# Performance work log

Measured on AMD Instinct MI355X. Metric: run time of the kernel, lower is better.

## Reference

```python
import jax, jax.numpy as jnp
import numpy as np

B, S, D, H, HD, L, V, FF = 4, 2048, 768, 12, 64, 6, 32000, 3072
EPS = 1e-5


def setup_inputs() -> dict:
    key = jax.random.key(0)
    ks = jax.random.split(key, 12)
    s = 0.02
    return {
        "input_ids": jax.random.randint(ks[0], (B, S), 0, V),
        "emb": jax.random.normal(ks[1], (V, D), jnp.float32) * s,
        "q_w": jax.random.normal(ks[2], (L, D, D), jnp.float32) * s,
        "q_b": jnp.zeros((L, D), jnp.float32),
        "k_w": jax.random.normal(ks[3], (L, D, D), jnp.float32) * s,
        "k_b": jnp.zeros((L, D), jnp.float32),
        "v_w": jax.random.normal(ks[4], (L, D, D), jnp.float32) * s,
        "v_b": jnp.zeros((L, D), jnp.float32),
        "o_w": jax.random.normal(ks[5], (L, D, D), jnp.float32) * s,
        "o_b": jnp.zeros((L, D), jnp.float32),
        "f1_w": jax.random.normal(ks[6], (L, D, FF), jnp.float32) * s,
        "f1_b": jnp.zeros((L, FF), jnp.float32),
        "f2_w": jax.random.normal(ks[7], (L, FF, D), jnp.float32) * s,
        "f2_b": jnp.zeros((L, D), jnp.float32),
        "n1_w": jnp.ones((L, D), jnp.float32),
        "n1_b": jnp.zeros((L, D), jnp.float32),
        "n2_w": jnp.ones((L, D), jnp.float32),
        "n2_b": jnp.zeros((L, D), jnp.float32),
        "fn_w": jnp.ones((D,), jnp.float32),
        "fn_b": jnp.zeros((D,), jnp.float32),
    }


def _ln(x, w, b):
    m = jnp.mean(x, axis=-1, keepdims=True)
    v = jnp.var(x, axis=-1, keepdims=True)
    return (x - m) * jax.lax.rsqrt(v + EPS) * w + b


def _rope(x):
    # x: [B, S, D]; RoPE applied on full embed dim (as in source)
    inv_freq = 1.0 / (10000.0 ** (jnp.arange(0, D, 2, dtype=jnp.float32) / D))
    ang = jnp.arange(x.shape[1], dtype=jnp.float32)[:, None] * inv_freq[None, :]  # [S, D/2]
    cos, sin = jnp.cos(ang), jnp.sin(ang)
    xe, xo = x[..., ::2], x[..., 1::2]
    re = xe * cos - xo * sin
    ro = xo * cos + xe * sin
    return jnp.stack([re, ro], axis=-1).reshape(x.shape)


def _forward(input_ids, emb, q_w, q_b, k_w, k_b, v_w, v_b, o_w, o_b,
             f1_w, f1_b, f2_w, f2_b, n1_w, n1_b, n2_w, n2_b, fn_w, fn_b):
    h = _rope(emb[input_ids])  # [B, S, D]
    scale = 1.0 / np.sqrt(HD)

    def block(h, p):
        (qw, qb, kw, kb, vw, vb, ow, ob, f1w, f1b, f2w, f2b,
         w1, b1, w2, b2) = p
        xn = _ln(h, w1, b1)
        q = (xn @ qw + qb).reshape(B, S, H, HD)
        k = (xn @ kw + kb).reshape(B, S, H, HD)
        v = (xn @ vw + vb).reshape(B, S, H, HD)
        scores = jnp.einsum('bqhd,bkhd->bhqk', q, k) * scale
        attn = jax.nn.softmax(scores, axis=-1)
        ctx = jnp.einsum('bhqk,bkhd->bqhd', attn, v).reshape(B, S, D)
        h = h + (ctx @ ow + ob)
        xn2 = _ln(h, w2, b2)
        ff = jax.nn.gelu(xn2 @ f1w + f1b, approximate=False) @ f2w + f2b
        return h + ff, None

    params = (q_w, q_b, k_w, k_b, v_w, v_b, o_w, o_b,
              f1_w, f1_b, f2_w, f2_b, n1_w, n1_b, n2_w, n2_b)
    h, _ = jax.lax.scan(block, h, params)
    h = _ln(h, fn_w, fn_b)
    return h @ emb.T  # tied output projection: [B, S, V]


def reference(input_ids, emb, q_w, q_b, k_w, k_b, v_w, v_b, o_w, o_b,
              f1_w, f1_b, f2_w, f2_b, n1_w, n1_b, n2_w, n2_b, fn_w, fn_b):
    return _forward(input_ids, emb, q_w, q_b, k_w, k_b, v_w, v_b, o_w, o_b,
                    f1_w, f1_b, f2_w, f2_b, n1_w, n1_b, n2_w, n2_b, fn_w, fn_b)
```

## Files before the change

kernel.cpp:

```cpp
#include <hip/hip_runtime.h>
#include <hip/hip_bf16.h>
#include <cstdint>
#include <cstddef>

#define TB 4
#define TS 2048
#define TD 768
#define TH 12
#define THD 64
#define TL 6
#define TV 32000
#define TFF 3072
#define TT (TB*TS)
#define TQKV 2304

typedef __bf16 bf16_t;
typedef __attribute__((ext_vector_type(8))) __bf16 bf16x8;
typedef __attribute__((ext_vector_type(4))) __bf16 bf16x4;
typedef __attribute__((ext_vector_type(4))) float f32x4;

__device__ __forceinline__ unsigned short f2bf(float f) {
  union { float f; unsigned u; } x; x.f = f;
  unsigned r = x.u + 0x7fffu + ((x.u >> 16) & 1u);
  return (unsigned short)(r >> 16);
}

__device__ __forceinline__ float fexp2(float x) {
  float r; asm("v_exp_f32 %0, %1" : "=v"(r) : "v"(x)); return r;
}

__device__ __forceinline__ void gld_lds16(const void* g, void* l) {
  unsigned loff = (unsigned)(uintptr_t)l;
  __builtin_amdgcn_global_load_lds(
      (const __attribute__((address_space(1))) unsigned int*)(uintptr_t)g,
      (__attribute__((address_space(3))) unsigned int*)(uintptr_t)loff, 16, 0, 0);
}

#define IRFENCE() asm volatile("" ::: "memory")

__global__ void embed_rope(const int* __restrict__ ids, const float* __restrict__ emb,
                           float* __restrict__ h) {
  int t = blockIdx.x;
  int s = t & (TS - 1);
  int id = ids[t];
  const float* row = emb + (size_t)id * TD;
  float* out = h + (size_t)t * TD;
  for (int p = threadIdx.x; p < TD/2; p += blockDim.x) {
    float xe = row[2*p], xo = row[2*p+1];
    float inv = expf(-(float)(2*p) * (9.210340371976184f / (float)TD));
    float ang = (float)s * inv;
    float c = cosf(ang), sn = sinf(ang);
    out[2*p]   = xe*c - xo*sn;
    out[2*p+1] = xo*c + xe*sn;
  }
}

__global__ __launch_bounds__(256) void ln_fwd(const float* __restrict__ x,
                                              const float* __restrict__ w,
                                              const float* __restrict__ b,
                                              unsigned short* __restrict__ y) {
  int row = blockIdx.x;
  const float* xr = x + (size_t)row * TD;
  int tid = threadIdx.x;
  float4 v = {0.f, 0.f, 0.f, 0.f};
  if (tid < 192) v = *(const float4*)(xr + tid*4);
  float s = (v.x+v.y)+(v.z+v.w);
  float q = (v.x*v.x+v.y*v.y)+(v.z*v.z+v.w*v.w);
  for (int o = 32; o; o >>= 1) { s += __shfl_down(s, o); q += __shfl_down(q, o); }
  __shared__ float ss[4], sq[4];
  int wave = tid >> 6, lane = tid & 63;
  if (lane == 0) { ss[wave] = s; sq[wave] = q; }
  __syncthreads();
  s = ss[0]+ss[1]+ss[2]+ss[3];
  q = sq[0]+sq[1]+sq[2]+sq[3];
  float mean = s * (1.0f/TD);
  float var  = q * (1.0f/TD) - mean*mean;
  float rstd = rsqrtf(var + 1e-5f);
  if (tid < 192) {
    const float4 wv = *(const float4*)(w + tid*4);
    const float4 bv = *(const float4*)(b + tid*4);
    ushort4 o4;
    o4.x = f2bf((v.x-mean)*rstd*wv.x + bv.x);
    o4.y = f2bf((v.y-mean)*rstd*wv.y + bv.y);
    o4.z = f2bf((v.z-mean)*rstd*wv.z + bv.z);
    o4.w = f2bf((v.w-mean)*rstd*wv.w + bv.w);
    *(ushort4*)(y + (size_t)row*TD + tid*4) = o4;
  }
}

__global__ __launch_bounds__(256) void transpose_to_bf16(const float* __restrict__ W,
                                                         unsigned short* __restrict__ Wt,
                                                         int K, int N, int row_off,
                                                         size_t lstride) {
  int ntn = N / 64;
  int tk = (blockIdx.x / ntn) * 64;
  int tn = (blockIdx.x % ntn) * 64;
  const float* Wb = W + (size_t)blockIdx.y * K * N;
  unsigned short* Ob = Wt + (size_t)blockIdx.y * lstride;
  __shared__ float tile[64][65];
  int tid = threadIdx.x;
  int c = tid & 63, w = tid >> 6;
  #pragma unroll
  for (int i = 0; i < 16; ++i) {
    int r = i*4 + w;
    tile[r][c] = Wb[(size_t)(tk + r) * N + tn + c];
  }
  __syncthreads();
  #pragma unroll
  for (int i = 0; i < 16; ++i) {
    int r = i*4 + w;
    Ob[(size_t)(row_off + tn + r) * K + tk + c] = f2bf(tile[c][r]);
  }
}

__global__ void pack_qkv_bias(const float* __restrict__ qb, const float* __restrict__ kb,
                              const float* __restrict__ vb, float* __restrict__ out) {
  int lay = blockIdx.x, i = threadIdx.x;
  out[lay*TQKV + i]        = qb[lay*TD + i];
  out[lay*TQKV + TD + i]   = kb[lay*TD + i];
  out[lay*TQKV + 2*TD + i] = vb[lay*TD + i];
}

__global__ void convert_bf16_k(const float* __restrict__ in, unsigned short* __restrict__ out) {
  size_t i = ((size_t)blockIdx.x * 256 + threadIdx.x) * 4;
  float4 v = *(const float4*)(in + i);
  ushort4 o;
  o.x = f2bf(v.x); o.y = f2bf(v.y); o.z = f2bf(v.z); o.w = f2bf(v.w);
  *(ushort4*)(out + i) = o;
}

template<int MODE>
__global__ __launch_bounds__(256, 2) void gemm_bt(
    const bf16_t* __restrict__ A, const bf16_t* __restrict__ Bt,
    const float* __restrict__ bias, void* __restrict__ out,
    void* __restrict__ out2,
    int N, int K, int ntn) {
  __shared__ __align__(16) bf16_t As[2][128*64];
  __shared__ __align__(16) bf16_t Bs[2][128*64];
  const int tid = threadIdx.x;
  const int lane = tid & 63;
  const int wave = tid >> 6;
  const int wm = wave >> 1, wn = wave & 1;
  const int nwg = gridDim.x;
  const int orig = blockIdx.x;
  const int qd = nwg >> 3, rr = nwg & 7;
  const int xcd = orig & 7, sub = orig >> 3;
  const int wg = (xcd < rr ? xcd*(qd+1) : rr*(qd+1) + (xcd-rr)*qd) + sub;
  const int tm = wg / ntn, tn = wg % ntn;
  const bf16_t* Ab = A + (size_t)tm * 128 * K;
  const bf16_t* Bb = Bt + (size_t)tn * 128 * K;
  const int lr = lane >> 3;
  const int lc = ((lane & 7) ^ lr) * 8;
  const int l15 = lane & 15, l4 = lane >> 4;
  const int flip = (l15 & 7) << 3;
  const int NT = K >> 6;
  f32x4 acc[4][4] = {};

#define STAGE(t, buf) do {                                                   \
    _Pragma("unroll")                                                        \
    for (int it = 0; it < 4; ++it) {                                         \
      const int r0 = it*32 + wave*8;                                         \
      gld_lds16(Ab + (size_t)(r0 + lr)*K + (t)*64 + lc, &As[buf][r0*64 + lr*64]); \
      gld_lds16(Bb + (size_t)(r0 + lr)*K + (t)*64 + lc, &Bs[buf][r0*64 + lr*64]); \
    }                                                                        \
  } while (0)

  STAGE(0, 0);
  for (int t = 0; t < NT; ++t) {
    const int cur = t & 1;
    if (t < NT - 1) {
      STAGE(t+1, cur^1);
      asm volatile("s_waitcnt vmcnt(8)" ::: "memory");
    } else {
      asm volatile("s_waitcnt vmcnt(0)" ::: "memory");
    }
    IRFENCE(); __builtin_amdgcn_s_barrier(); IRFENCE();
    #pragma unroll
    for (int kh = 0; kh < 2; ++kh) {
      bf16x8 af[4], bfr[4];
      #pragma unroll
      for (int i = 0; i < 4; ++i)
        af[i] = *(const bf16x8*)&As[cur][(wm*64 + i*16 + l15)*64 + ((kh*32 + l4*8) ^ flip)];
      #pragma unroll
      for (int i = 0; i < 4; ++i)
        bfr[i] = *(const bf16x8*)&Bs[cur][(wn*64 + i*16 + l15)*64 + ((kh*32 + l4*8) ^ flip)];
      #pragma unroll
      for (int mi = 0; mi < 4; ++mi)
        #pragma unroll
        for (int ni = 0; ni < 4; ++ni)
          acc[mi][ni] = __builtin_amdgcn_mfma_f32_16x16x32_bf16(af[mi], bfr[ni], acc[mi][ni], 0, 0, 0);
    }
    IRFENCE(); __builtin_amdgcn_s_barrier(); IRFENCE();
  }
#undef STAGE
  const int rb = tm*128 + wm*64 + l4*4;
  const int cbase = tn*128 + wn*64 + l15;
  const bool vsec = (MODE == 4) && (tn >= (2*TD)/128);
  #pragma unroll
  for (int mi = 0; mi < 4; ++mi) {
    #pragma unroll
    for (int ni = 0; ni < 4; ++ni) {
      const int c = cbase + ni*16;
      const float bv = (MODE == 3) ? 0.0f : bias[c];
      if (MODE == 4 && vsec) {
        const int cc = c - 2*TD;
        const int hh = cc >> 6, d = cc & 63;
        const int row0 = rb + mi*16;
        const int bidx = row0 >> 11, s = row0 & (TS-1);
        ushort4 o4;
        o4.x = f2bf(acc[mi][ni][0] + bv);
        o4.y = f2bf(acc[mi][ni][1] + bv);
        o4.z = f2bf(acc[mi][ni][2] + bv);
        o4.w = f2bf(acc[mi][ni][3] + bv);
        *(ushort4*)((unsigned short*)out2 + ((size_t)(bidx*TH + hh)*THD + d)*TS + s) = o4;
        continue;
      }
      #pragma unroll
      for (int r = 0; r < 4; ++r) {
        const size_t idx = (size_t)(rb + mi*16 + r) * N + c;
        float vv = acc[mi][ni][r] + bv;
        if (MODE == 0 || MODE == 4) {
          ((unsigned short*)out)[idx] = f2bf(vv);
        } else if (MODE == 1) {
          vv = 0.5f * vv * (1.0f + erff(vv * 0.70710678118654752f));
          ((unsigned short*)out)[idx] = f2bf(vv);
        } else if (MODE == 2) {
          ((float*)out)[idx] += vv;
        } else {
          ((float*)out)[idx] = vv;
        }
      }
    }
  }
}

__device__ __forceinline__ int lds_half_off(int R, int C) {
  int lin = ((((R >> 4) << 1) | (C >> 5)) << 10) | ((R & 15) << 6) | ((C & 31) << 1);
  return lin ^ (((R >> 3) & 1) << 5);
}

template<int MODE>
__global__ __launch_bounds__(512, 2) void gemm256(
    const bf16_t* __restrict__ A, const bf16_t* __restrict__ Bt,
    const float* __restrict__ bias, void* __restrict__ out,
    int N, int K, int ntn) {
  __shared__ __align__(16) bf16_t lds[2][2][2][8192];
  const int tid = threadIdx.x;
  const int lane = tid & 63;
  const int wave = tid >> 6;
  const int wm = wave >> 2;
  const int wn = wave & 3;
  const int orig = blockIdx.x;
  const int grp = orig >> 8;
  const int rem = orig & 255;
  const int tn = grp*8 + (rem >> 5);
  const int tm = rem & 31;
  const bf16_t* Ab = A  + (size_t)tm * 256 * K;
  const bf16_t* Bb = Bt + (size_t)tn * 256 * K;
  const int l15 = lane & 15, l4 = lane >> 4;
  const int s_row = wave*16 + (lane >> 2);
  const int s_col0 = ((lane & 3) * 8) ^ ((lane >= 32) ? 16 : 0);
  const int NT = K >> 6;

  f32x4 acc[2][4][2][2] = {};
  bf16x8 afr[4][2], bfr0[2][2], bfr1[2][2];

#define STAGEH(mat, half, kt, buf) do {                                          \
    const bf16_t* base_ = (mat) ? Bb : Ab;                                       \
    _Pragma("unroll")                                                            \
    for (int j_ = 0; j_ < 2; ++j_)                                               \
      gld_lds16(base_ + (size_t)((half)*128 + s_row)*K + (kt)*64 + j_*32 + s_col0, \
                &lds[buf][mat][half][(wave*2 + j_) * 512]);                      \
  } while (0)
#define RDA(buf, half) do {                                                      \
    _Pragma("unroll")                                                            \
    for (int m4_ = 0; m4_ < 4; ++m4_)                                            \
      _Pragma("unroll")                                                          \
      for (int kh_ = 0; kh_ < 2; ++kh_)                                          \
        afr[m4_][kh_] = *(const bf16x8*)((const char*)&lds[buf][0][half][0] +    \
            lds_half_off(wm*64 + m4_*16 + l15, kh_*32 + l4*8));                  \
  } while (0)
#define RDB(buf, half, dst) do {                                                 \
    _Pragma("unroll")                                                            \
    for (int n2_ = 0; n2_ < 2; ++n2_)                                            \
      _Pragma("unroll")                                                          \
      for (int kh_ = 0; kh_ < 2; ++kh_)                                          \
        dst[n2_][kh_] = *(const bf16x8*)((const char*)&lds[buf][1][half][0] +    \
            lds_half_off(wn*32 + n2_*16 + l15, kh_*32 + l4*8));                  \
  } while (0)
#define MMA(hA, hB, bsrc) do {                                                   \
    __builtin_amdgcn_s_setprio(1);                                               \
    _Pragma("unroll")                                                            \
    for (int m4_ = 0; m4_ < 4; ++m4_)                                            \
      _Pragma("unroll")                                                          \
      for (int n2_ = 0; n2_ < 2; ++n2_)                                          \
        _Pragma("unroll")                                                        \
        for (int kh_ = 0; kh_ < 2; ++kh_)                                        \
          acc[hA][m4_][hB][n2_] = __builtin_amdgcn_mfma_f32_16x16x32_bf16(       \
              afr[m4_][kh_], bsrc[n2_][kh_], acc[hA][m4_][hB][n2_], 0, 0, 0);    \
    __builtin_amdgcn_s_setprio(0);                                               \
  } while (0)
#define WAITV(n)  asm volatile("s_waitcnt vmcnt(" #n ")" ::: "memory")
#define GATE()    do { asm volatile("s_waitcnt lgkmcnt(0)" ::: "memory");        \
                       __builtin_amdgcn_sched_barrier(0); } while (0)
#define BAR()     do { IRFENCE(); __builtin_amdgcn_s_barrier(); IRFENCE(); } while (0)

  STAGEH(0, 0, 0, 0);
  STAGEH(1, 0, 0, 0);
  STAGEH(1, 1, 0, 0);
  STAGEH(0, 1, 0, 0);
  WAITV(4);
  BAR();

  for (int t = 0; t < NT; ++t) {
    const int c = t & 1;
    const bool last = (t == NT - 1);
    RDA(c, 0);
    RDB(c, 0, bfr0);
    if (!last) STAGEH(0, 0, t+1, c^1);
    if (last) WAITV(2); else WAITV(4);
    BAR(); GATE();
    MMA(0, 0, bfr0);
    RDB(c, 1, bfr1);
    if (!last) STAGEH(1, 0, t+1, c^1);
    if (last) WAITV(0); else WAITV(4);
    BAR(); GATE();
    MMA(0, 1, bfr1);
    RDA(c, 1);
    if (!last) STAGEH(1, 1, t+1, c^1);
    BAR(); GATE();
    MMA(1, 0, bfr0);
    if (!last) STAGEH(0, 1, t+1, c^1);
    WAITV(4);
    BAR(); GATE();
    MMA(1, 1, bfr1);
  }

  #pragma unroll
  for (int hA = 0; hA < 2; ++hA)
    #pragma unroll
    for (int m4 = 0; m4 < 4; ++m4) {
      const int row = tm*256 + hA*128 + wm*64 + m4*16 + l4*4;
      #pragma unroll
      for (int hB = 0; hB < 2; ++hB)
        #pragma unroll
        for (int n2 = 0; n2 < 2; ++n2) {
          const int col = tn*256 + hB*128 + wn*32 + n2*16 + l15;
          const float bv = (MODE == 3) ? 0.0f : bias[col];
          #pragma unroll
          for (int r = 0; r < 4; ++r) {
            const size_t idx = (size_t)(row + r) * N + col;
            float vv = acc[hA][m4][hB][n2][r] + bv;
            if (MODE == 0) {
              ((unsigned short*)out)[idx] = f2bf(vv);
            } else if (MODE == 1) {
              vv = 0.5f * vv * (1.0f + erff(vv * 0.70710678118654752f));
              ((unsigned short*)out)[idx] = f2bf(vv);
            } else if (MODE == 2) {
              ((float*)out)[idx] += vv;
            } else {
              ((float*)out)[idx] = vv;
            }
          }
        }
    }
#undef STAGEH
#undef RDA
#undef RDB
#undef MMA
#undef WAITV
#undef GATE
#undef BAR
}

__global__ __launch_bounds__(256, 4) void attn_fwd(
    const bf16_t* __restrict__ xqkv, const bf16_t* __restrict__ vt,
    unsigned short* __restrict__ ctx) {
  __shared__ __align__(16) bf16_t Ks[2][64*64];
  __shared__ __align__(16) bf16_t Vs[2][64*64];
  __shared__ __align__(16) bf16_t pl[4][16*64];
  const int tid = threadIdx.x, lane = tid & 63, wave = tid >> 6;
  const int orig = blockIdx.x;
  const int wg = (orig & 7) * 96 + (orig >> 3);
  const int qb16 = wg & 15;
  const int bh = wg >> 4;
  const int b = bh / TH, h = bh % TH;
  const bf16_t* qp = xqkv + (size_t)b*TS*TQKV + h*THD;
  const bf16_t* kp = xqkv + (size_t)b*TS*TQKV + TD + h*THD;
  const bf16_t* vp = vt + (size_t)bh*THD*TS;
  const int l15 = lane & 15, l4 = lane >> 4;
  const int qrow0 = qb16*128 + wave*32;
  const float C1 = 0.18033688011112042f;
  bf16x8 qf[2][2];
  #pragma unroll
  for (int mi = 0; mi < 2; ++mi)
    #pragma unroll
    for (int kh = 0; kh < 2; ++kh)
      qf[mi][kh] = *(const bf16x8*)(qp + (size_t)(qrow0 + mi*16 + l15)*TQKV + kh*32 + l4*8);
  const int srow = lane >> 3;
  const int scol = ((lane & 7) ^ srow) * 8;
  f32x4 o[2][4] = {};
  float rm[2] = {-1e30f, -1e30f}, rl[2] = {0.0f, 0.0f};
  const int flipw = (l15 & 7) << 3;

  #define STAGE(t, buf) do {                                                     \
    _Pragma("unroll")                                                            \
    for (int i_ = 0; i_ < 2; ++i_) {                                             \
      const int r_ = i_*32 + wave*8;                                             \
      gld_lds16(kp + (size_t)((t)*64 + r_ + srow)*TQKV + scol, &Ks[buf][r_*64]); \
      gld_lds16(vp + (size_t)(r_ + srow)*TS + (t)*64 + scol,   &Vs[buf][r_*64]); \
    }                                                                            \
  } while (0)

  STAGE(0, 0);
  for (int t = 0; t < TS/64; ++t) {
    const int cur = t & 1;
    if (t < TS/64 - 1) {
      STAGE(t+1, cur^1);
      asm volatile("s_waitcnt vmcnt(4)" ::: "memory");
    } else {
      asm volatile("s_waitcnt vmcnt(0)" ::: "memory");
    }
    IRFENCE(); __builtin_amdgcn_s_barrier(); IRFENCE();
    f32x4 st[2][4] = {};
    #pragma unroll
    for (int nj = 0; nj < 4; ++nj) {
      const int row = nj*16 + l15;
      const int flip = (row & 7) << 3;
      bf16x8 kf0 = *(const bf16x8*)&Ks[cur][row*64 + ((l4*8) ^ flip)];
      bf16x8 kf1 = *(const bf16x8*)&Ks[cur][row*64 + ((32 + l4*8) ^ flip)];
      st[0][nj] = __builtin_amdgcn_mfma_f32_16x16x32_bf16(kf0, qf[0][0], st[0][nj], 0, 0, 0);
      st[0][nj] = __builtin_amdgcn_mfma_f32_16x16x32_bf16(kf1, qf[0][1], st[0][nj], 0, 0, 0);
      st[1][nj] = __builtin_amdgcn_mfma_f32_16x16x32_bf16(kf0, qf[1][0], st[1][nj], 0, 0, 0);
      st[1][nj] = __builtin_amdgcn_mfma_f32_16x16x32_bf16(kf1, qf[1][1], st[1][nj], 0, 0, 0);
    }
    float mx[2];
    #pragma unroll
    for (int mi = 0; mi < 2; ++mi) {
      float m0 = fmaxf(fmaxf(st[mi][0][0], st[mi][0][1]), fmaxf(st[mi][0][2], st[mi][0][3]));
      float m1 = fmaxf(fmaxf(st[mi][1][0], st[mi][1][1]), fmaxf(st[mi][1][2], st[mi][1][3]));
      float m2 = fmaxf(fmaxf(st[mi][2][0], st[mi][2][1]), fmaxf(st[mi][2][2], st[mi][2][3]));
      float m3 = fmaxf(fmaxf(st[mi][3][0], st[mi][3][1]), fmaxf(st[mi][3][2], st[mi][3][3]));
      float m = fmaxf(fmaxf(m0, m1), fmaxf(m2, m3)) * C1;
      m = fmaxf(m, __shfl_xor(m, 16));
      m = fmaxf(m, __shfl_xor(m, 32));
      mx[mi] = m;
    }
    float worst = fmaxf(mx[0] - rm[0], mx[1] - rm[1]);
    if (!__all(worst <= 11.54f)) {
      #pragma unroll
      for (int mi = 0; mi < 2; ++mi) {
        float mn = fmaxf(rm[mi], mx[mi]);
        float sc = fexp2(rm[mi] - mn);
        rm[mi] = mn;
        rl[mi] *= sc;
        #pragma unroll
        for (int r = 0; r < 4; ++r) {
          float scr = __shfl(sc, l4*4 + r, 16);
          #pragma unroll
          for (int df = 0; df < 4; ++df) o[mi][df][r] *= scr;
        }
      }
    }
    bf16x8 pa[2][2];
    #pragma unroll
    for (int mi = 0; mi < 2; ++mi) {
      float rs = 0.0f;
      #pragma unroll
      for (int nj = 0; nj < 4; ++nj) {
        float p0 = fexp2(st[mi][nj][0]*C1 - rm[mi]);
        float p1 = fexp2(st[mi][nj][1]*C1 - rm[mi]);
        float p2 = fexp2(st[mi][nj][2]*C1 - rm[mi]);
        float p3 = fexp2(st[mi][nj][3]*C1 - rm[mi]);
        rs += (p0+p1)+(p2+p3);
        bf16x4 pk;
        pk[0] = (bf16_t)p0; pk[1] = (bf16_t)p1; pk[2] = (bf16_t)p2; pk[3] = (bf16_t)p3;
        const int colb = (nj*16 + l4*4) ^ flipw;
        *(bf16x4*)(&pl[wave][l15*64 + colb]) = pk;
      }
      rs += __shfl_xor(rs, 16);
      rs += __shfl_xor(rs, 32);
      rl[mi] += rs;
      pa[mi][0] = *(const bf16x8*)&pl[wave][l15*64 + ((l4*8) ^ flipw)];
      pa[mi][1] = *(const bf16x8*)&pl[wave][l15*64 + ((32 + l4*8) ^ flipw)];
    }
    #pragma unroll
    for (int df = 0; df < 4; ++df) {
      const int vrow = df*16 + l15;
      const int flip = (vrow & 7) << 3;
      bf16x8 vf0 = *(const bf16x8*)&Vs[cur][vrow*64 + ((l4*8) ^ flip)];
      bf16x8 vf1 = *(const bf16x8*)&Vs[cur][vrow*64 + ((32 + l4*8) ^ flip)];
      o[0][df] = __builtin_amdgcn_mfma_f32_16x16x32_bf16(pa[0][0], vf0, o[0][df], 0, 0, 0);
      o[0][df] = __builtin_amdgcn_mfma_f32_16x16x32_bf16(pa[0][1], vf1, o[0][df], 0, 0, 0);
      o[1][df] = __builtin_amdgcn_mfma_f32_16x16x32_bf16(pa[1][0], vf0, o[1][df], 0, 0, 0);
      o[1][df] = __builtin_amdgcn_mfma_f32_16x16x32_bf16(pa[1][1], vf1, o[1][df], 0, 0, 0);
    }
    IRFENCE(); __builtin_amdgcn_s_barrier(); IRFENCE();
  }
  #undef STAGE
  #pragma unroll
  for (int mi = 0; mi < 2; ++mi) {
    const float inv = 1.0f / rl[mi];
    #pragma unroll
    for (int r = 0; r < 4; ++r) {
      const float invr = __shfl(inv, l4*4 + r, 16);
      const size_t rowoff = (size_t)b*TS*TD + (size_t)(qrow0 + mi*16 + l4*4 + r)*TD + h*THD;
      #pragma unroll
      for (int df = 0; df < 4; ++df)
        ctx[rowoff + df*16 + l15] = f2bf(o[mi][df][r] * invr);
    }
  }
}

extern "C" void kernel_launch(void* const* d_in, const int* in_sizes, int n_in,
                              void* d_out, int out_size, void* d_ws, size_t ws_size,
                              hipStream_t stream) {
  (void)in_sizes; (void)n_in; (void)out_size;
  const int*   ids  = (const int*)  d_in[0];
  const float* emb  = (const float*)d_in[1];
  const float* q_w  = (const float*)d_in[2];
  const float* q_b  = (const float*)d_in[3];
  const float* k_w  = (const float*)d_in[4];
  const float* k_b  = (const float*)d_in[5];
  const float* v_w  = (const float*)d_in[6];
  const float* v_b  = (const float*)d_in[7];
  const float* o_w  = (const float*)d_in[8];
  const float* o_b  = (const float*)d_in[9];
  const float* f1_w = (const float*)d_in[10];
  const float* f1_b = (const float*)d_in[11];
  const float* f2_w = (const float*)d_in[12];
  const float* f2_b = (const float*)d_in[13];
  const float* n1_w = (const float*)d_in[14];
  const float* n1_b = (const float*)d_in[15];
  const float* n2_w = (const float*)d_in[16];
  const float* n2_b = (const float*)d_in[17];
  const float* fn_w = (const float*)d_in[18];
  const float* fn_b = (const float*)d_in[19];

  char* ws = (char*)d_ws;
  size_t off = 0;
  auto alloc = [&](size_t bytes) -> void* {
    void* p = ws + off;
    off += (bytes + 255) & ~(size_t)255;
    return p;
  };
  float*          h    = (float*)         alloc((size_t)TT*TD*4);
  unsigned short* xn   = (unsigned short*)alloc((size_t)TT*TD*2);
  unsigned short* xqkv = (unsigned short*)alloc((size_t)TT*TQKV*2);
  unsigned short* cb   = (unsigned short*)alloc((size_t)TT*TD*2);
  unsigned short* ffb  = (unsigned short*)alloc((size_t)TT*TFF*2);
  unsigned short* wqkv = (unsigned short*)alloc((size_t)TL*TQKV*TD*2);
  unsigned short* wot  = (unsigned short*)alloc((size_t)TL*TD*TD*2);
  unsigned short* wf1t = (unsigned short*)alloc((size_t)TL*TD*TFF*2);
  unsigned short* wf2t = (unsigned short*)alloc((size_t)TL*TD*TFF*2);
  unsigned short* embb = (unsigned short*)alloc((size_t)TV*TD*2);
  float*          bqkv = (float*)         alloc((size_t)TL*TQKV*4);
  if (off > ws_size) return;
  bf16_t* vt = (bf16_t*)ffb;

  transpose_to_bf16<<<dim3((TD/64)*(TD/64), TL), 256, 0, stream>>>(q_w, wqkv, TD, TD, 0,    (size_t)TQKV*TD);
  transpose_to_bf16<<<dim3((TD/64)*(TD/64), TL), 256, 0, stream>>>(k_w, wqkv, TD, TD, TD,   (size_t)TQKV*TD);
  transpose_to_bf16<<<dim3((TD/64)*(TD/64), TL), 256, 0, stream>>>(v_w, wqkv, TD, TD, 2*TD, (size_t)TQKV*TD);
  transpose_to_bf16<<<dim3((TD/64)*(TD/64), TL), 256, 0, stream>>>(o_w, wot, TD, TD, 0, (size_t)TD*TD);
  transpose_to_bf16<<<dim3((TD/64)*(TFF/64), TL), 256, 0, stream>>>(f1_w, wf1t, TD, TFF, 0, (size_t)TD*TFF);
  transpose_to_bf16<<<dim3((TFF/64)*(TD/64), TL), 256, 0, stream>>>(f2_w, wf2t, TFF, TD, 0, (size_t)TD*TFF);
  pack_qkv_bias<<<TL, TD, 0, stream>>>(q_b, k_b, v_b, bqkv);
  convert_bf16_k<<<(TV*TD)/1024, 256, 0, stream>>>(emb, embb);
  embed_rope<<<TT, 256, 0, stream>>>(ids, emb, h);

  for (int lay = 0; lay < TL; ++lay) {
    ln_fwd<<<TT, 256, 0, stream>>>(h, n1_w + lay*TD, n1_b + lay*TD, xn);
    gemm_bt<4><<<(TT/128)*(TQKV/128), 256, 0, stream>>>((const bf16_t*)xn,
        (const bf16_t*)(wqkv + (size_t)lay*TQKV*TD), bqkv + lay*TQKV, xqkv, vt, TQKV, TD, TQKV/128);
    attn_fwd<<<TB*TH*(TS/128), 256, 0, stream>>>((const bf16_t*)xqkv, vt, cb);
    gemm_bt<2><<<(TT/128)*(TD/128), 256, 0, stream>>>((const bf16_t*)cb,
        (const bf16_t*)(wot + (size_t)lay*TD*TD), o_b + lay*TD, h, nullptr, TD, TD, TD/128);
    ln_fwd<<<TT, 256, 0, stream>>>(h, n2_w + lay*TD, n2_b + lay*TD, xn);
    gemm_bt<1><<<(TT/128)*(TFF/128), 256, 0, stream>>>((const bf16_t*)xn,
        (const bf16_t*)(wf1t + (size_t)lay*TD*TFF), f1_b + lay*TFF, ffb, nullptr, TFF, TD, TFF/128);
    gemm_bt<2><<<(TT/128)*(TD/128), 256, 0, stream>>>((const bf16_t*)ffb,
        (const bf16_t*)(wf2t + (size_t)lay*TD*TFF), f2_b + lay*TD, h, nullptr, TD, TFF, TD/128);
  }
  ln_fwd<<<TT, 256, 0, stream>>>(h, fn_w, fn_b, xn);
  gemm256<3><<<32*(TV/256), 512, 0, stream>>>((const bf16_t*)xn,
      (const bf16_t*)embb, nullptr, d_out, TV, TD, TV/256);
}
```

Before: 2.427 ms.

## Split-K the FF2 GEMM and fuse residual adds into LayerNorm kernels

The FF2 GEMM (K=3072, only 384 tiles) now runs split-K over 4 slices and writes bf16 partials. A new ln_fused kernel sums those partials, adds the bias and the residual into h, then applies the next LayerNorm. The O-projection likewise writes bf16 output that ln_fused adds to the residual, replacing the fp32 read-modify-write epilogues. The aim is more parallelism for the low-occupancy FF2 GEMM and fewer passes over h, at the cost of extra partial-buffer traffic and bf16 rounding of the residual contributions.

```diff
diff --git a/kernel.cpp b/kernel.cpp
--- a/kernel.cpp
+++ b/kernel.cpp
@@ -23,6 +23,9 @@
   union { float f; unsigned u; } x; x.f = f;
   unsigned r = x.u + 0x7fffu + ((x.u >> 16) & 1u);
   return (unsigned short)(r >> 16);
+}
+__device__ __forceinline__ float bf2f(unsigned short u) {
+  union { unsigned u; float f; } x; x.u = (unsigned)u << 16; return x.f;
 }
 
 __device__ __forceinline__ float fexp2(float x) {
@@ -88,6 +91,52 @@
   }
 }
 
+template<int NPART>
+__global__ __launch_bounds__(256) void ln_fused(
+    float* __restrict__ hbuf, const unsigned short* __restrict__ parts,
+    const float* __restrict__ pbias,
+    const float* __restrict__ w, const float* __restrict__ b,
+    unsigned short* __restrict__ y) {
+  int row = blockIdx.x;
+  int tid = threadIdx.x;
+  float4 v = {0.f, 0.f, 0.f, 0.f};
+  if (tid < 192) {
+    v = *(const float4*)(hbuf + (size_t)row*TD + tid*4);
+    #pragma unroll
+    for (int p = 0; p < NPART; ++p) {
+      ushort4 u = *(const ushort4*)(parts + (size_t)p*TT*TD + (size_t)row*TD + tid*4);
+      v.x += bf2f(u.x); v.y += bf2f(u.y); v.z += bf2f(u.z); v.w += bf2f(u.w);
+    }
+    if (pbias) {
+      float4 pb = *(const float4*)(pbias + tid*4);
+      v.x += pb.x; v.y += pb.y; v.z += pb.z; v.w += pb.w;
+    }
+  }
+  float s = (v.x+v.y)+(v.z+v.w);
+  float q = (v.x*v.x+v.y*v.y)+(v.z*v.z+v.w*v.w);
+  for (int o = 32; o; o >>= 1) { s += __shfl_down(s, o); q += __shfl_down(q, o); }
+  __shared__ float ss[4], sq[4];
+  int wave = tid >> 6, lane = tid & 63;
+  if (lane == 0) { ss[wave] = s; sq[wave] = q; }
+  __syncthreads();
+  s = ss[0]+ss[1]+ss[2]+ss[3];
+  q = sq[0]+sq[1]+sq[2]+sq[3];
+  float mean = s * (1.0f/TD);
+  float var  = q * (1.0f/TD) - mean*mean;
+  float rstd = rsqrtf(var + 1e-5f);
+  if (tid < 192) {
+    *(float4*)(hbuf + (size_t)row*TD + tid*4) = v;
+    const float4 wv = *(const float4*)(w + tid*4);
+    const float4 bv = *(const float4*)(b + tid*4);
+    ushort4 o4;
+    o4.x = f2bf((v.x-mean)*rstd*wv.x + bv.x);
+    o4.y = f2bf((v.y-mean)*rstd*wv.y + bv.y);
+    o4.z = f2bf((v.z-mean)*rstd*wv.z + bv.z);
+    o4.w = f2bf((v.w-mean)*rstd*wv.w + bv.w);
+    *(ushort4*)(y + (size_t)row*TD + tid*4) = o4;
+  }
+}
+
 __global__ __launch_bounds__(256) void transpose_to_bf16(const float* __restrict__ W,
                                                          unsigned short* __restrict__ Wt,
                                                          int K, int N, int row_off,
@@ -147,13 +196,16 @@
   const int xcd = orig & 7, sub = orig >> 3;
   const int wg = (xcd < rr ? xcd*(qd+1) : rr*(qd+1) + (xcd-rr)*qd) + sub;
   const int tm = wg / ntn, tn = wg % ntn;
-  const bf16_t* Ab = A + (size_t)tm * 128 * K;
-  const bf16_t* Bb = Bt + (size_t)tn * 128 * K;
+  const int nslice = (MODE == 5) ? 4 : 1;
+  const int ks = (MODE == 5) ? blockIdx.y : 0;
+  const int koff = ks * (K / nslice);
+  const bf16_t* Ab = A + (size_t)tm * 128 * K + koff;
+  const bf16_t* Bb = Bt + (size_t)tn * 128 * K + koff;
   const int lr = lane >> 3;
   const int lc = ((lane & 7) ^ lr) * 8;
   const int l15 = lane & 15, l4 = lane >> 4;
   const int flip = (l15 & 7) << 3;
-  const int NT = K >> 6;
+  const int NT = K / (64 * nslice);
   f32x4 acc[4][4] = {};
 
 #define STAGE(t, buf) do {                                                   \
@@ -201,7 +253,7 @@
     #pragma unroll
     for (int ni = 0; ni < 4; ++ni) {
       const int c = cbase + ni*16;
-      const float bv = (MODE == 3) ? 0.0f : bias[c];
+      const float bv = (MODE == 3 || MODE == 5) ? 0.0f : bias[c];
       if (MODE == 4 && vsec) {
         const int cc = c - 2*TD;
         const int hh = cc >> 6, d = cc & 63;
@@ -226,6 +278,8 @@
           ((unsigned short*)out)[idx] = f2bf(vv);
         } else if (MODE == 2) {
           ((float*)out)[idx] += vv;
+        } else if (MODE == 5) {
+          ((unsigned short*)out)[(size_t)ks*TT*TD + idx] = f2bf(vv);
         } else {
           ((float*)out)[idx] = vv;
         }
@@ -549,6 +603,7 @@
   unsigned short* xqkv = (unsigned short*)alloc((size_t)TT*TQKV*2);
   unsigned short* cb   = (unsigned short*)alloc((size_t)TT*TD*2);
   unsigned short* ffb  = (unsigned short*)alloc((size_t)TT*TFF*2);
+  unsigned short* cpart= (unsigned short*)alloc((size_t)4*TT*TD*2);
   unsigned short* wqkv = (unsigned short*)alloc((size_t)TL*TQKV*TD*2);
   unsigned short* wot  = (unsigned short*)alloc((size_t)TL*TD*TD*2);
   unsigned short* wf1t = (unsigned short*)alloc((size_t)TL*TD*TFF*2);
@@ -568,20 +623,25 @@
   convert_bf16_k<<<(TV*TD)/1024, 256, 0, stream>>>(emb, embb);
   embed_rope<<<TT, 256, 0, stream>>>(ids, emb, h);
 
+  ln_fwd<<<TT, 256, 0, stream>>>(h, n1_w, n1_b, xn);
   for (int lay = 0; lay < TL; ++lay) {
-    ln_fwd<<<TT, 256, 0, stream>>>(h, n1_w + lay*TD, n1_b + lay*TD, xn);
     gemm_bt<4><<<(TT/128)*(TQKV/128), 256, 0, stream>>>((const bf16_t*)xn,
         (const bf16_t*)(wqkv + (size_t)lay*TQKV*TD), bqkv + lay*TQKV, xqkv, vt, TQKV, TD, TQKV/128);
     attn_fwd<<<TB*TH*(TS/128), 256, 0, stream>>>((const bf16_t*)xqkv, vt, cb);
-    gemm_bt<2><<<(TT/128)*(TD/128), 256, 0, stream>>>((const bf16_t*)cb,
-        (const bf16_t*)(wot + (size_t)lay*TD*TD), o_b + lay*TD, h, nullptr, TD, TD, TD/128);
-    ln_fwd<<<TT, 256, 0, stream>>>(h, n2_w + lay*TD, n2_b + lay*TD, xn);
+    gemm_bt<0><<<(TT/128)*(TD/128), 256, 0, stream>>>((const bf16_t*)cb,
+        (const bf16_t*)(wot + (size_t)lay*TD*TD), o_b + lay*TD, xn, nullptr, TD, TD, TD/128);
+    ln_fused<1><<<TT, 256, 0, stream>>>(h, xn, nullptr, n2_w + lay*TD, n2_b + lay*TD, xn);
     gemm_bt<1><<<(TT/128)*(TFF/128), 256, 0, stream>>>((const bf16_t*)xn,
         (const bf16_t*)(wf1t + (size_t)lay*TD*TFF), f1_b + lay*TFF, ffb, nullptr, TFF, TD, TFF/128);
-    gemm_bt<2><<<(TT/128)*(TD/128), 256, 0, stream>>>((const bf16_t*)ffb,
-        (const bf16_t*)(wf2t + (size_t)lay*TD*TFF), f2_b + lay*TD, h, nullptr, TD, TFF, TD/128);
-  }
-  ln_fwd<<<TT, 256, 0, stream>>>(h, fn_w, fn_b, xn);
+    gemm_bt<5><<<dim3((TT/128)*(TD/128), 4), 256, 0, stream>>>((const bf16_t*)ffb,
+        (const bf16_t*)(wf2t + (size_t)lay*TD*TFF), nullptr, cpart, nullptr, TD, TFF, TD/128);
+    if (lay < TL - 1) {
+      ln_fused<4><<<TT, 256, 0, stream>>>(h, cpart, f2_b + lay*TD,
+          n1_w + (lay+1)*TD, n1_b + (lay+1)*TD, xn);
+    } else {
+      ln_fused<4><<<TT, 256, 0, stream>>>(h, cpart, f2_b + lay*TD, fn_w, fn_b, xn);
+    }
+  }
   gemm256<3><<<32*(TV/256), 512, 0, stream>>>((const bf16_t*)xn,
       (const bf16_t*)embb, nullptr, d_out, TV, TD, TV/256);
 }
```

Result: faster. 2.325 ms (-4.2%).
